# Performance work log

Measured on AMD Instinct MI355X. Metric: run time of the kernel, lower is better.

The kernel has to match this reference:

```python
import jax, jax.numpy as jnp
import numpy as np

H = 1024      # hidden_size
I = 2816      # intermediate_size
E = 8         # num_experts
TOP_K = 2     # num_experts_per_tok


def setup_inputs() -> dict:
    key = jax.random.key(0)
    ks = jax.random.split(key, 5)
    s = 0.02
    return {
        "hidden_states": jax.random.normal(ks[0], (2, 1024, H), dtype=jnp.float32),
        "router_w": jax.random.normal(ks[1], (E, H), dtype=jnp.float32) * s,   # nn.Linear(H, E): [out, in]
        "gate_w": jax.random.normal(ks[2], (E, I, H), dtype=jnp.float32) * s,  # stacked gate_proj [I, H]
        "up_w": jax.random.normal(ks[3], (E, I, H), dtype=jnp.float32) * s,    # stacked up_proj [I, H]
        "down_w": jax.random.normal(ks[4], (E, H, I), dtype=jnp.float32) * s,  # stacked down_proj [H, I]
    }


def _moe(hidden_states, router_w, gate_w, up_w, down_w):
    B, S, Hd = hidden_states.shape
    x = hidden_states.reshape(-1, Hd)                       # [T, H]
    logits = x @ router_w.T                                 # [T, E]
    probs = jax.nn.softmax(logits.astype(jnp.float32), axis=-1)
    top_w, top_idx = jax.lax.top_k(probs, TOP_K)            # [T, K] (NOT renormalized, per Jamba)
    top_w = top_w.astype(x.dtype)
    # per-(token, expert) combine weight: sum_k top_w[t,k] * [top_idx[t,k]==e]
    onehot = jax.nn.one_hot(top_idx, E, dtype=x.dtype)      # [T, K, E]
    w_te = jnp.einsum('tk,tke->te', top_w, onehot)          # [T, E]
    # dense per-expert gated MLP, combined by routing weights (zero for unselected)
    g = jnp.einsum('th,eih->tei', x, gate_w)                # [T, E, I]
    u = jnp.einsum('th,eih->tei', x, up_w)
    h = jax.nn.silu(g) * u                                  # [T, E, I]
    y = jnp.einsum('tei,ehi,te->th', h, down_w, w_te)       # [T, H]
    return y.reshape(B, S, Hd)


def reference(hidden_states, router_w, gate_w, up_w, down_w):
    return _moe(hidden_states, router_w, gate_w, up_w, down_w)
```

## Files before the change

kernel.cpp:

```cpp
#include <hip/hip_runtime.h>
#include <stdint.h>
#include <stddef.h>

#define Hdim 1024
#define Idim 2816
#define Edim 8
#define Tdim 2048

typedef short bf16x8 __attribute__((ext_vector_type(8)));
typedef float f32x4 __attribute__((ext_vector_type(4)));

#define WS_CNT   0
#define WS_OFFS  64
#define WS_TOK   1024
#define WS_W     66560
#define WS_XBF   132096
#define WS_H     4326400

__device__ __forceinline__ unsigned short f2bf(float f) {
  unsigned int u = __builtin_bit_cast(unsigned int, f);
  u += 0x7fffu + ((u >> 16) & 1u);
  return (unsigned short)(u >> 16);
}

__device__ __forceinline__ void async16(const void* g, void* l) {
  __builtin_amdgcn_global_load_lds(
      (const __attribute__((address_space(1))) void*)g,
      (__attribute__((address_space(3))) void*)l, 16, 0, 0);
}

__global__ __launch_bounds__(256) void router_kernel(
    const float* __restrict__ x, const float* __restrict__ rw,
    int* __restrict__ cnt, int* __restrict__ tok_slot,
    float* __restrict__ w_slot, unsigned short* __restrict__ xbf)
{
  const int wave = threadIdx.x >> 6;
  const int lane = threadIdx.x & 63;
  const int t = blockIdx.x * 4 + wave;

  float acc[Edim];
#pragma unroll
  for (int e = 0; e < Edim; ++e) acc[e] = 0.f;
  const float* xr = x + (size_t)t * Hdim;
#pragma unroll
  for (int i = 0; i < Hdim / 64; ++i) {
    int idx = i * 64 + lane;
    float v = xr[idx];
    xbf[(size_t)t * Hdim + idx] = f2bf(v);
#pragma unroll
    for (int e = 0; e < Edim; ++e) acc[e] = fmaf(v, rw[e * Hdim + idx], acc[e]);
  }
#pragma unroll
  for (int e = 0; e < Edim; ++e) {
    float a = acc[e];
#pragma unroll
    for (int s = 32; s >= 1; s >>= 1) a += __shfl_xor(a, s, 64);
    acc[e] = a;
  }
  if (lane == 0) {
    float mx = acc[0];
#pragma unroll
    for (int e = 1; e < Edim; ++e) mx = fmaxf(mx, acc[e]);
    float p[Edim], se = 0.f;
#pragma unroll
    for (int e = 0; e < Edim; ++e) { p[e] = __expf(acc[e] - mx); se += p[e]; }
    float inv = 1.f / se;
#pragma unroll
    for (int e = 0; e < Edim; ++e) p[e] *= inv;
    int e1 = 0; float p1 = p[0];
#pragma unroll
    for (int e = 1; e < Edim; ++e) if (p[e] > p1) { p1 = p[e]; e1 = e; }
    int e2 = -1; float p2 = -1.f;
#pragma unroll
    for (int e = 0; e < Edim; ++e) if (e != e1 && p[e] > p2) { p2 = p[e]; e2 = e; }
    int pos1 = atomicAdd(&cnt[e1], 1);
    tok_slot[e1 * Tdim + pos1] = t; w_slot[e1 * Tdim + pos1] = p1;
    int pos2 = atomicAdd(&cnt[e2], 1);
    tok_slot[e2 * Tdim + pos2] = t; w_slot[e2 * Tdim + pos2] = p2;
  }
}

__global__ void offs_kernel(const int* __restrict__ cnt, int* __restrict__ offs)
{
  if (threadIdx.x == 0 && blockIdx.x == 0) {
    int s = 0;
    for (int e = 0; e < Edim; ++e) { offs[e] = s; s += cnt[e]; }
  }
}

__global__ __launch_bounds__(256) void gateup_kernel(
    const unsigned short* __restrict__ xbf,
    const float* __restrict__ gw, const float* __restrict__ uw,
    const int* __restrict__ cnt, const int* __restrict__ offs,
    const int* __restrict__ tok_slot, unsigned short* __restrict__ hbuf)
{
  const int e = blockIdx.z, mtile = blockIdx.y, ntile = blockIdx.x;
  const int n_e = cnt[e];
  if (mtile * 128 >= n_e) return;

  __shared__ unsigned short Al[2][128][32];
  __shared__ unsigned short Bgl[2][64][32];
  __shared__ unsigned short Bul[2][64][32];
  __shared__ int toks[128];

  const int tid = threadIdx.x;
  const int wave = tid >> 6, lane = tid & 63;
  const int wr = (wave >> 1) * 64, wc = (wave & 1) * 32;

  if (tid < 128) {
    int r = mtile * 128 + tid;
    toks[tid] = tok_slot[e * Tdim + ((r < n_e) ? r : mtile * 128)];
  }
  __syncthreads();

  const int br = tid >> 2, bc = tid & 3;
  const float* gbase = gw + ((size_t)e * Idim + (size_t)ntile * 64 + br) * Hdim + bc * 8;
  const float* ubase = uw + ((size_t)e * Idim + (size_t)ntile * 64 + br) * Hdim + bc * 8;

  f32x4 accg[4][2], accu[4][2];
#pragma unroll
  for (int m = 0; m < 4; ++m)
#pragma unroll
    for (int n = 0; n < 2; ++n) {
      f32x4 z = {0.f, 0.f, 0.f, 0.f};
      accg[m][n] = z; accu[m][n] = z;
    }

  f32x4 bg0, bg1, bu0, bu1;
  auto loadB = [&](int kt) {
    const float* gp = gbase + (size_t)kt * 32;
    const float* up = ubase + (size_t)kt * 32;
    bg0 = *(const f32x4*)gp; bg1 = *(const f32x4*)(gp + 4);
    bu0 = *(const f32x4*)up; bu1 = *(const f32x4*)(up + 4);
  };
  auto writeB = [&](int buf) {
    bf16x8 vg, vu;
#pragma unroll
    for (int j = 0; j < 4; ++j) {
      vg[j] = (short)f2bf(bg0[j]); vg[j + 4] = (short)f2bf(bg1[j]);
      vu[j] = (short)f2bf(bu0[j]); vu[j + 4] = (short)f2bf(bu1[j]);
    }
    *(bf16x8*)&Bgl[buf][br][bc * 8] = vg;
    *(bf16x8*)&Bul[buf][br][bc * 8] = vu;
  };
  auto stageA = [&](int buf, int kt) {
#pragma unroll
    for (int ii = 0; ii < 2; ++ii) {
      int i = wave + ii * 4;
      int row = i * 16 + (lane >> 2);
      int t = toks[row];
      const unsigned short* g = xbf + (size_t)t * Hdim + kt * 32 + (lane & 3) * 8;
      async16(g, &Al[buf][i * 16][0]);
    }
  };
  auto compute = [&](int buf) {
    bf16x8 af[4], bgf[2], buff[2];
#pragma unroll
    for (int m = 0; m < 4; ++m)
      af[m] = *(const bf16x8*)&Al[buf][wr + m * 16 + (lane & 15)][(lane >> 4) * 8];
#pragma unroll
    for (int n = 0; n < 2; ++n) {
      bgf[n] = *(const bf16x8*)&Bgl[buf][wc + n * 16 + (lane & 15)][(lane >> 4) * 8];
      buff[n] = *(const bf16x8*)&Bul[buf][wc + n * 16 + (lane & 15)][(lane >> 4) * 8];
    }
#pragma unroll
    for (int m = 0; m < 4; ++m)
#pragma unroll
      for (int n = 0; n < 2; ++n) {
        accg[m][n] = __builtin_amdgcn_mfma_f32_16x16x32_bf16(af[m], bgf[n], accg[m][n], 0, 0, 0);
        accu[m][n] = __builtin_amdgcn_mfma_f32_16x16x32_bf16(af[m], buff[n], accu[m][n], 0, 0, 0);
      }
  };

  loadB(0); stageA(0, 0); writeB(0);
  __syncthreads();
  int cur = 0;
  for (int kt = 0; kt < Hdim / 32 - 1; ++kt) {
    loadB(kt + 1);
    stageA(cur ^ 1, kt + 1);
    compute(cur);
    writeB(cur ^ 1);
    __syncthreads();
    cur ^= 1;
  }
  compute(cur);

  const size_t hb = (size_t)offs[e];
#pragma unroll
  for (int m = 0; m < 4; ++m)
#pragma unroll
    for (int n = 0; n < 2; ++n)
#pragma unroll
      for (int j = 0; j < 4; ++j) {
        int r = wr + m * 16 + ((lane >> 4) << 2) + j;
        int gr = mtile * 128 + r;
        if (gr < n_e) {
          int col = ntile * 64 + wc + n * 16 + (lane & 15);
          float g = accg[m][n][j], u = accu[m][n][j];
          float s = g / (1.f + __expf(-g));
          hbuf[(hb + (size_t)gr) * Idim + col] = f2bf(s * u);
        }
      }
}

__global__ __launch_bounds__(256) void down_kernel(
    const unsigned short* __restrict__ hbuf, const float* __restrict__ dw,
    const int* __restrict__ cnt, const int* __restrict__ offs,
    const int* __restrict__ tok_slot, const float* __restrict__ w_slot,
    float* __restrict__ out)
{
  const int e = blockIdx.z, mtile = blockIdx.y, ntile = blockIdx.x;
  const int n_e = cnt[e];
  if (mtile * 128 >= n_e) return;
  const int off_e = offs[e];

  __shared__ unsigned short Al[2][128][32];
  __shared__ unsigned short Bl[2][64][32];
  __shared__ int toks[128];
  __shared__ float wts[128];

  const int tid = threadIdx.x;
  const int wave = tid >> 6, lane = tid & 63;
  const int wr = (wave >> 1) * 64, wc = (wave & 1) * 32;

  if (tid < 128) {
    int r = mtile * 128 + tid;
    int rc = (r < n_e) ? r : mtile * 128;
    toks[tid] = tok_slot[e * Tdim + rc];
    wts[tid]  = w_slot[e * Tdim + rc];
  }
  __syncthreads();

  const int br = tid >> 2, bc = tid & 3;
  const float* dbase = dw + ((size_t)e * Hdim + (size_t)ntile * 64 + br) * Idim + bc * 8;

  f32x4 acc[4][2];
#pragma unroll
  for (int m = 0; m < 4; ++m)
#pragma unroll
    for (int n = 0; n < 2; ++n) { f32x4 z = {0.f, 0.f, 0.f, 0.f}; acc[m][n] = z; }

  f32x4 b0, b1;
  auto loadB = [&](int kt) {
    const float* p = dbase + (size_t)kt * 32;
    b0 = *(const f32x4*)p; b1 = *(const f32x4*)(p + 4);
  };
  auto writeB = [&](int buf) {
    bf16x8 v;
#pragma unroll
    for (int j = 0; j < 4; ++j) { v[j] = (short)f2bf(b0[j]); v[j + 4] = (short)f2bf(b1[j]); }
    *(bf16x8*)&Bl[buf][br][bc * 8] = v;
  };
  auto stageA = [&](int buf, int kt) {
#pragma unroll
    for (int ii = 0; ii < 2; ++ii) {
      int i = wave + ii * 4;
      int row = i * 16 + (lane >> 2);
      int gr = mtile * 128 + row;
      int grc = (gr < n_e) ? gr : mtile * 128;
      const unsigned short* g = hbuf + (size_t)(off_e + grc) * Idim + kt * 32 + (lane & 3) * 8;
      async16(g, &Al[buf][i * 16][0]);
    }
  };
  auto compute = [&](int buf) {
    bf16x8 af[4], bf[2];
#pragma unroll
    for (int m = 0; m < 4; ++m)
      af[m] = *(const bf16x8*)&Al[buf][wr + m * 16 + (lane & 15)][(lane >> 4) * 8];
#pragma unroll
    for (int n = 0; n < 2; ++n)
      bf[n] = *(const bf16x8*)&Bl[buf][wc + n * 16 + (lane & 15)][(lane >> 4) * 8];
#pragma unroll
    for (int m = 0; m < 4; ++m)
#pragma unroll
      for (int n = 0; n < 2; ++n)
        acc[m][n] = __builtin_amdgcn_mfma_f32_16x16x32_bf16(af[m], bf[n], acc[m][n], 0, 0, 0);
  };

  loadB(0); stageA(0, 0); writeB(0);
  __syncthreads();
  int cur = 0;
  for (int kt = 0; kt < Idim / 32 - 1; ++kt) {
    loadB(kt + 1);
    stageA(cur ^ 1, kt + 1);
    compute(cur);
    writeB(cur ^ 1);
    __syncthreads();
    cur ^= 1;
  }
  compute(cur);

#pragma unroll
  for (int m = 0; m < 4; ++m)
#pragma unroll
    for (int n = 0; n < 2; ++n)
#pragma unroll
      for (int j = 0; j < 4; ++j) {
        int r = wr + m * 16 + ((lane >> 4) << 2) + j;
        int gr = mtile * 128 + r;
        if (gr < n_e) {
          int col = ntile * 64 + wc + n * 16 + (lane & 15);
          float v = acc[m][n][j] * wts[r];
          atomicAdd(out + (size_t)toks[r] * Hdim + col, v);
        }
      }
}

extern "C" void kernel_launch(void* const* d_in, const int* in_sizes, int n_in,
                              void* d_out, int out_size, void* d_ws, size_t ws_size,
                              hipStream_t stream) {
  const float* x  = (const float*)d_in[0];
  const float* rw = (const float*)d_in[1];
  const float* gw = (const float*)d_in[2];
  const float* uw = (const float*)d_in[3];
  const float* dw = (const float*)d_in[4];
  float* out = (float*)d_out;

  char* ws = (char*)d_ws;
  int*   cnt  = (int*)(ws + WS_CNT);
  int*   offs = (int*)(ws + WS_OFFS);
  int*   tok  = (int*)(ws + WS_TOK);
  float* wsl  = (float*)(ws + WS_W);
  unsigned short* xbf  = (unsigned short*)(ws + WS_XBF);
  unsigned short* hbuf = (unsigned short*)(ws + WS_H);

  hipMemsetAsync(cnt, 0, 64, stream);
  hipMemsetAsync(out, 0, (size_t)out_size * sizeof(float), stream);

  router_kernel<<<Tdim / 4, 256, 0, stream>>>(x, rw, cnt, tok, wsl, xbf);
  offs_kernel<<<1, 64, 0, stream>>>(cnt, offs);
  gateup_kernel<<<dim3(Idim / 64, Tdim / 128, Edim), 256, 0, stream>>>(
      xbf, gw, uw, cnt, offs, tok, hbuf);
  down_kernel<<<dim3(Hdim / 64, Tdim / 128, Edim), 256, 0, stream>>>(
      hbuf, dw, cnt, offs, tok, wsl, out);
}
```

Baseline: 542.3 us.

## Use fragment-major LDS layout, K=64 down tiles, and separate combine kernel

Shared-memory tiles now use a fragment-major layout, so each lane reads its MFMA operand contiguously, which should cut LDS bank conflicts. The down kernel doubles its K step to 64 to halve barrier and loop overhead. It also drops the per-element fp32 atomicAdd scatter and the output memset: down results go to a bf16 per-slot buffer, and a new combine kernel gathers each token's two expert rows and applies the routing weights. This adds an extra kernel launch and an extra round-trip of intermediate data, and rounding the down outputs to bf16 adds precision loss.

```diff
diff --git a/kernel.cpp b/kernel.cpp
--- a/kernel.cpp
+++ b/kernel.cpp
@@ -9,20 +9,26 @@
 
 typedef short bf16x8 __attribute__((ext_vector_type(8)));
 typedef float f32x4 __attribute__((ext_vector_type(4)));
+typedef unsigned short us4 __attribute__((ext_vector_type(4)));
 
 #define WS_CNT   0
 #define WS_OFFS  64
 #define WS_TOK   1024
 #define WS_W     66560
-#define WS_XBF   132096
-#define WS_H     4326400
+#define WS_MAP   132096
+#define WS_XBF   148480
+#define WS_H     4342784
+#define WS_Y     27411456
 
 __device__ __forceinline__ unsigned short f2bf(float f) {
   unsigned int u = __builtin_bit_cast(unsigned int, f);
   u += 0x7fffu + ((u >> 16) & 1u);
   return (unsigned short)(u >> 16);
 }
-
+__device__ __forceinline__ float bf2f(unsigned short h) {
+  unsigned int u = ((unsigned int)h) << 16;
+  return __builtin_bit_cast(float, u);
+}
 __device__ __forceinline__ void async16(const void* g, void* l) {
   __builtin_amdgcn_global_load_lds(
       (const __attribute__((address_space(1))) void*)g,
@@ -32,7 +38,8 @@
 __global__ __launch_bounds__(256) void router_kernel(
     const float* __restrict__ x, const float* __restrict__ rw,
     int* __restrict__ cnt, int* __restrict__ tok_slot,
-    float* __restrict__ w_slot, unsigned short* __restrict__ xbf)
+    float* __restrict__ w_slot, int* __restrict__ tokmap,
+    unsigned short* __restrict__ xbf)
 {
   const int wave = threadIdx.x >> 6;
   const int lane = threadIdx.x & 63;
@@ -75,8 +82,10 @@
     for (int e = 0; e < Edim; ++e) if (e != e1 && p[e] > p2) { p2 = p[e]; e2 = e; }
     int pos1 = atomicAdd(&cnt[e1], 1);
     tok_slot[e1 * Tdim + pos1] = t; w_slot[e1 * Tdim + pos1] = p1;
+    tokmap[t] = e1 * Tdim + pos1;
     int pos2 = atomicAdd(&cnt[e2], 1);
     tok_slot[e2 * Tdim + pos2] = t; w_slot[e2 * Tdim + pos2] = p2;
+    tokmap[Tdim + t] = e2 * Tdim + pos2;
   }
 }
 
@@ -98,24 +107,27 @@
   const int n_e = cnt[e];
   if (mtile * 128 >= n_e) return;
 
-  __shared__ unsigned short Al[2][128][32];
-  __shared__ unsigned short Bgl[2][64][32];
-  __shared__ unsigned short Bul[2][64][32];
+  __shared__ unsigned short A [2][8][64][8];
+  __shared__ unsigned short Bg[2][4][64][8];
+  __shared__ unsigned short Bu[2][4][64][8];
   __shared__ int toks[128];
 
   const int tid = threadIdx.x;
   const int wave = tid >> 6, lane = tid & 63;
   const int wr = (wave >> 1) * 64, wc = (wave & 1) * 32;
+  const int wr16 = (wave >> 1) * 4, wc16 = (wave & 1) * 2;
 
   if (tid < 128) {
     int r = mtile * 128 + tid;
-    toks[tid] = tok_slot[e * Tdim + ((r < n_e) ? r : mtile * 128)];
+    toks[tid] = tok_slot[e * Tdim + ((r < n_e) ? r : (n_e - 1))];
   }
   __syncthreads();
 
   const int br = tid >> 2, bc = tid & 3;
   const float* gbase = gw + ((size_t)e * Idim + (size_t)ntile * 64 + br) * Hdim + bc * 8;
   const float* ubase = uw + ((size_t)e * Idim + (size_t)ntile * 64 + br) * Hdim + bc * 8;
+  const int bslot = bc * 16 + (br & 15);
+  const int bgrp  = br >> 4;
 
   f32x4 accg[4][2], accu[4][2];
 #pragma unroll
@@ -140,35 +152,34 @@
       vg[j] = (short)f2bf(bg0[j]); vg[j + 4] = (short)f2bf(bg1[j]);
       vu[j] = (short)f2bf(bu0[j]); vu[j + 4] = (short)f2bf(bu1[j]);
     }
-    *(bf16x8*)&Bgl[buf][br][bc * 8] = vg;
-    *(bf16x8*)&Bul[buf][br][bc * 8] = vu;
+    *(bf16x8*)&Bg[buf][bgrp][bslot][0] = vg;
+    *(bf16x8*)&Bu[buf][bgrp][bslot][0] = vu;
   };
   auto stageA = [&](int buf, int kt) {
 #pragma unroll
     for (int ii = 0; ii < 2; ++ii) {
-      int i = wave + ii * 4;
-      int row = i * 16 + (lane >> 2);
-      int t = toks[row];
-      const unsigned short* g = xbf + (size_t)t * Hdim + kt * 32 + (lane & 3) * 8;
-      async16(g, &Al[buf][i * 16][0]);
+      int mb = wave + ii * 4;
+      int t = toks[mb * 16 + (lane & 15)];
+      const unsigned short* g = xbf + (size_t)t * Hdim + kt * 32 + (lane >> 4) * 8;
+      async16(g, &A[buf][mb][0][0]);
     }
   };
   auto compute = [&](int buf) {
-    bf16x8 af[4], bgf[2], buff[2];
+    bf16x8 af[4], bgf[2], buf_[2];
 #pragma unroll
     for (int m = 0; m < 4; ++m)
-      af[m] = *(const bf16x8*)&Al[buf][wr + m * 16 + (lane & 15)][(lane >> 4) * 8];
+      af[m] = *(const bf16x8*)&A[buf][wr16 + m][lane][0];
 #pragma unroll
     for (int n = 0; n < 2; ++n) {
-      bgf[n] = *(const bf16x8*)&Bgl[buf][wc + n * 16 + (lane & 15)][(lane >> 4) * 8];
-      buff[n] = *(const bf16x8*)&Bul[buf][wc + n * 16 + (lane & 15)][(lane >> 4) * 8];
+      bgf[n] = *(const bf16x8*)&Bg[buf][wc16 + n][lane][0];
+      buf_[n] = *(const bf16x8*)&Bu[buf][wc16 + n][lane][0];
     }
 #pragma unroll
     for (int m = 0; m < 4; ++m)
 #pragma unroll
       for (int n = 0; n < 2; ++n) {
         accg[m][n] = __builtin_amdgcn_mfma_f32_16x16x32_bf16(af[m], bgf[n], accg[m][n], 0, 0, 0);
-        accu[m][n] = __builtin_amdgcn_mfma_f32_16x16x32_bf16(af[m], buff[n], accu[m][n], 0, 0, 0);
+        accu[m][n] = __builtin_amdgcn_mfma_f32_16x16x32_bf16(af[m], buf_[n], accu[m][n], 0, 0, 0);
       }
   };
 
@@ -206,33 +217,29 @@
 __global__ __launch_bounds__(256) void down_kernel(
     const unsigned short* __restrict__ hbuf, const float* __restrict__ dw,
     const int* __restrict__ cnt, const int* __restrict__ offs,
-    const int* __restrict__ tok_slot, const float* __restrict__ w_slot,
-    float* __restrict__ out)
+    unsigned short* __restrict__ ybuf)
 {
   const int e = blockIdx.z, mtile = blockIdx.y, ntile = blockIdx.x;
   const int n_e = cnt[e];
   if (mtile * 128 >= n_e) return;
   const int off_e = offs[e];
 
-  __shared__ unsigned short Al[2][128][32];
-  __shared__ unsigned short Bl[2][64][32];
-  __shared__ int toks[128];
-  __shared__ float wts[128];
+  __shared__ unsigned short A [2][16][64][8];
+  __shared__ unsigned short Bl[2][8][64][8];
 
   const int tid = threadIdx.x;
   const int wave = tid >> 6, lane = tid & 63;
   const int wr = (wave >> 1) * 64, wc = (wave & 1) * 32;
-
-  if (tid < 128) {
-    int r = mtile * 128 + tid;
-    int rc = (r < n_e) ? r : mtile * 128;
-    toks[tid] = tok_slot[e * Tdim + rc];
-    wts[tid]  = w_slot[e * Tdim + rc];
-  }
-  __syncthreads();
-
-  const int br = tid >> 2, bc = tid & 3;
-  const float* dbase = dw + ((size_t)e * Hdim + (size_t)ntile * 64 + br) * Idim + bc * 8;
+  const int wr16 = (wave >> 1) * 4, wc2 = (wave & 1) * 2;
+
+  const int br = tid >> 2, kq = tid & 3;
+  const float* dbase = dw + ((size_t)e * Hdim + (size_t)ntile * 64 + br) * Idim + kq * 16;
+  const int k0 = kq * 16;
+  const int g0 = (br >> 4) * 2 + (k0 >> 5);
+  const int l0 = (((k0 & 31) >> 3) << 4) + (br & 15);
+  const int k1 = k0 + 8;
+  const int g1 = (br >> 4) * 2 + (k1 >> 5);
+  const int l1 = (((k1 & 31) >> 3) << 4) + (br & 15);
 
   f32x4 acc[4][2];
 #pragma unroll
@@ -240,47 +247,61 @@
 #pragma unroll
     for (int n = 0; n < 2; ++n) { f32x4 z = {0.f, 0.f, 0.f, 0.f}; acc[m][n] = z; }
 
-  f32x4 b0, b1;
+  f32x4 b0, b1, b2, b3;
   auto loadB = [&](int kt) {
-    const float* p = dbase + (size_t)kt * 32;
-    b0 = *(const f32x4*)p; b1 = *(const f32x4*)(p + 4);
+    const float* p = dbase + (size_t)kt * 64;
+    b0 = *(const f32x4*)p;        b1 = *(const f32x4*)(p + 4);
+    b2 = *(const f32x4*)(p + 8);  b3 = *(const f32x4*)(p + 12);
   };
   auto writeB = [&](int buf) {
-    bf16x8 v;
-#pragma unroll
-    for (int j = 0; j < 4; ++j) { v[j] = (short)f2bf(b0[j]); v[j + 4] = (short)f2bf(b1[j]); }
-    *(bf16x8*)&Bl[buf][br][bc * 8] = v;
+    bf16x8 v0, v1;
+#pragma unroll
+    for (int j = 0; j < 4; ++j) {
+      v0[j] = (short)f2bf(b0[j]); v0[j + 4] = (short)f2bf(b1[j]);
+      v1[j] = (short)f2bf(b2[j]); v1[j + 4] = (short)f2bf(b3[j]);
+    }
+    *(bf16x8*)&Bl[buf][g0][l0][0] = v0;
+    *(bf16x8*)&Bl[buf][g1][l1][0] = v1;
   };
   auto stageA = [&](int buf, int kt) {
 #pragma unroll
     for (int ii = 0; ii < 2; ++ii) {
-      int i = wave + ii * 4;
-      int row = i * 16 + (lane >> 2);
-      int gr = mtile * 128 + row;
-      int grc = (gr < n_e) ? gr : mtile * 128;
-      const unsigned short* g = hbuf + (size_t)(off_e + grc) * Idim + kt * 32 + (lane & 3) * 8;
-      async16(g, &Al[buf][i * 16][0]);
+      int mb = wave + ii * 4;
+      int gr = mtile * 128 + mb * 16 + (lane & 15);
+      int rc = (gr < n_e) ? gr : (n_e - 1);
+#pragma unroll
+      for (int kc = 0; kc < 2; ++kc) {
+        const unsigned short* g = hbuf + (size_t)(off_e + rc) * Idim
+                                + (size_t)kt * 64 + kc * 32 + (lane >> 4) * 8;
+        async16(g, &A[buf][mb * 2 + kc][0][0]);
+      }
     }
   };
   auto compute = [&](int buf) {
-    bf16x8 af[4], bf[2];
+    bf16x8 af[4][2], bfr[2][2];
 #pragma unroll
     for (int m = 0; m < 4; ++m)
-      af[m] = *(const bf16x8*)&Al[buf][wr + m * 16 + (lane & 15)][(lane >> 4) * 8];
+#pragma unroll
+      for (int kk = 0; kk < 2; ++kk)
+        af[m][kk] = *(const bf16x8*)&A[buf][(wr16 + m) * 2 + kk][lane][0];
 #pragma unroll
     for (int n = 0; n < 2; ++n)
-      bf[n] = *(const bf16x8*)&Bl[buf][wc + n * 16 + (lane & 15)][(lane >> 4) * 8];
+#pragma unroll
+      for (int kk = 0; kk < 2; ++kk)
+        bfr[n][kk] = *(const bf16x8*)&Bl[buf][(wc2 + n) * 2 + kk][lane][0];
 #pragma unroll
     for (int m = 0; m < 4; ++m)
 #pragma unroll
       for (int n = 0; n < 2; ++n)
-        acc[m][n] = __builtin_amdgcn_mfma_f32_16x16x32_bf16(af[m], bf[n], acc[m][n], 0, 0, 0);
+#pragma unroll
+        for (int kk = 0; kk < 2; ++kk)
+          acc[m][n] = __builtin_amdgcn_mfma_f32_16x16x32_bf16(af[m][kk], bfr[n][kk], acc[m][n], 0, 0, 0);
   };
 
   loadB(0); stageA(0, 0); writeB(0);
   __syncthreads();
   int cur = 0;
-  for (int kt = 0; kt < Idim / 32 - 1; ++kt) {
+  for (int kt = 0; kt < Idim / 64 - 1; ++kt) {
     loadB(kt + 1);
     stageA(cur ^ 1, kt + 1);
     compute(cur);
@@ -300,10 +321,28 @@
         int gr = mtile * 128 + r;
         if (gr < n_e) {
           int col = ntile * 64 + wc + n * 16 + (lane & 15);
-          float v = acc[m][n][j] * wts[r];
-          atomicAdd(out + (size_t)toks[r] * Hdim + col, v);
+          ybuf[(size_t)(off_e + gr) * Hdim + col] = f2bf(acc[m][n][j]);
         }
       }
+}
+
+__global__ __launch_bounds__(256) void combine_kernel(
+    const unsigned short* __restrict__ ybuf, const int* __restrict__ offs,
+    const int* __restrict__ tokmap, const float* __restrict__ w_slot,
+    float* __restrict__ out)
+{
+  const int t = blockIdx.x;
+  const int i1 = tokmap[t], i2 = tokmap[Tdim + t];
+  const float w1 = w_slot[i1], w2 = w_slot[i2];
+  const int s1 = offs[i1 >> 11] + (i1 & (Tdim - 1));
+  const int s2 = offs[i2 >> 11] + (i2 & (Tdim - 1));
+  const int c = threadIdx.x * 4;
+  us4 a = *(const us4*)&ybuf[(size_t)s1 * Hdim + c];
+  us4 b = *(const us4*)&ybuf[(size_t)s2 * Hdim + c];
+  f32x4 r;
+#pragma unroll
+  for (int j = 0; j < 4; ++j) r[j] = w1 * bf2f(a[j]) + w2 * bf2f(b[j]);
+  *(f32x4*)&out[(size_t)t * Hdim + c] = r;
 }
 
 extern "C" void kernel_launch(void* const* d_in, const int* in_sizes, int n_in,
@@ -321,16 +360,18 @@
   int*   offs = (int*)(ws + WS_OFFS);
   int*   tok  = (int*)(ws + WS_TOK);
   float* wsl  = (float*)(ws + WS_W);
+  int*   map  = (int*)(ws + WS_MAP);
   unsigned short* xbf  = (unsigned short*)(ws + WS_XBF);
   unsigned short* hbuf = (unsigned short*)(ws + WS_H);
+  unsigned short* ybuf = (unsigned short*)(ws + WS_Y);
 
   hipMemsetAsync(cnt, 0, 64, stream);
-  hipMemsetAsync(out, 0, (size_t)out_size * sizeof(float), stream);
-
-  router_kernel<<<Tdim / 4, 256, 0, stream>>>(x, rw, cnt, tok, wsl, xbf);
+
+  router_kernel<<<Tdim / 4, 256, 0, stream>>>(x, rw, cnt, tok, wsl, map, xbf);
   offs_kernel<<<1, 64, 0, stream>>>(cnt, offs);
   gateup_kernel<<<dim3(Idim / 64, Tdim / 128, Edim), 256, 0, stream>>>(
       xbf, gw, uw, cnt, offs, tok, hbuf);
   down_kernel<<<dim3(Hdim / 64, Tdim / 128, Edim), 256, 0, stream>>>(
-      hbuf, dw, cnt, offs, tok, wsl, out);
-}
+      hbuf, dw, cnt, offs, ybuf);
+  combine_kernel<<<Tdim, 256, 0, stream>>>(ybuf, offs, map, wsl, out);
+}
```

New measurement: 497.7 us. -8.2%, faster.
